# Optimization experiments

Measured on AMD Instinct MI355X. Metric: run time of the kernel, lower is better.

## Reference

```python
import jax, jax.numpy as jnp
import numpy as np

C = 1024
FACTOR = 4
C_INT = C * FACTOR


def setup_inputs() -> dict:
    key = jax.random.key(0)
    ks = jax.random.split(key, 6)
    act = jax.random.normal(ks[0], (4, 2048, C), dtype=jnp.float32)
    mask = jnp.ones((4, 2048), dtype=jnp.float32)
    # LayerNorm params
    ln_scale = jnp.ones((C,), dtype=jnp.float32)
    ln_bias = jnp.zeros((C,), dtype=jnp.float32)
    # Linear 1 (init='linear'): lecun-normal-ish
    w1 = jax.random.normal(ks[1], (C, C_INT), dtype=jnp.float32) / np.sqrt(C)
    b1 = jnp.zeros((C_INT,), dtype=jnp.float32)
    # Linear 2 (init='final' -> zeros in AF2; use small random so grads are nontrivial)
    w2 = jax.random.normal(ks[2], (C_INT, C), dtype=jnp.float32) * 0.02
    b2 = jnp.zeros((C,), dtype=jnp.float32)
    return {"act": act, "mask": mask, "ln_scale": ln_scale, "ln_bias": ln_bias,
            "w1": w1, "b1": b1, "w2": w2, "b2": b2}


def _layernorm(x, scale, bias, eps=1e-5):
    mu = jnp.mean(x, axis=-1, keepdims=True)
    var = jnp.mean(jnp.square(x - mu), axis=-1, keepdims=True)
    return (x - mu) * jax.lax.rsqrt(var + eps) * scale + bias


def reference(act, mask, ln_scale, ln_bias, w1, b1, w2, b2):
    # mask is accepted but unused, matching the original forward.
    x = _layernorm(act, ln_scale, ln_bias)
    h = jax.nn.relu(jnp.einsum('bsc,cf->bsf', x, w1) + b1)
    return jnp.einsum('bsf,fc->bsc', h, w2) + b2
```

## Files before the change

kernel.cpp:

```cpp
#include <hip/hip_runtime.h>
#include <hip/hip_bf16.h>
#include <cstdint>

typedef unsigned short u16;
typedef __bf16 bf16x8 __attribute__((ext_vector_type(8)));
typedef float floatx4 __attribute__((ext_vector_type(4)));

#define AS1 __attribute__((address_space(1)))
#define AS3 __attribute__((address_space(3)))

static __device__ __forceinline__ u16 f2bf(float f) {
    union { float f; unsigned int u; } v; v.f = f;
    unsigned int u = v.u;
    return (u16)((u + 0x7FFFu + ((u >> 16) & 1u)) >> 16);
}

__device__ __forceinline__ void transpose_body(
    const float* __restrict__ in, u16* __restrict__ out,
    int R, int Ccols, int bx, int by, int tid, float (*tile)[33])
{
    const int tx = tid & 31;
    const int ty = tid >> 5;
    const int c0 = bx * 32;
    const int r0 = by * 32;
#pragma unroll
    for (int i = 0; i < 32; i += 8)
        tile[ty + i][tx] = in[(size_t)(r0 + ty + i) * Ccols + (c0 + tx)];
    __syncthreads();
#pragma unroll
    for (int i = 0; i < 32; i += 8)
        out[(size_t)(c0 + ty + i) * R + (r0 + tx)] = f2bf(tile[tx][ty + i]);
}

__global__ __launch_bounds__(256)
void prep(const float* __restrict__ w1, const float* __restrict__ w2,
          const float* __restrict__ act, const float* __restrict__ ln_scale,
          const float* __restrict__ ln_bias,
          u16* __restrict__ W1t, u16* __restrict__ W2t, u16* __restrict__ X)
{
    __shared__ float smem[32][33];
    const int id  = blockIdx.x;
    const int tid = threadIdx.x;

    if (id < 4096) {
        transpose_body(w1, W1t, 1024, 4096, id & 127, id >> 7, tid, smem);
        return;
    }
    if (id < 8192) {
        const int t = id - 4096;
        transpose_body(w2, W2t, 4096, 1024, t & 31, t >> 5, tid, smem);
        return;
    }
    const int row = id - 8192;
    const float4 v = ((const float4*)(act + (size_t)row * 1024))[tid];
    float s  = v.x + v.y + v.z + v.w;
    float ss = v.x * v.x + v.y * v.y + v.z * v.z + v.w * v.w;
#pragma unroll
    for (int off = 32; off > 0; off >>= 1) {
        s  += __shfl_xor(s, off, 64);
        ss += __shfl_xor(ss, off, 64);
    }
    float* red = &smem[0][0];
    const int wave = tid >> 6, lane = tid & 63;
    if (lane == 0) { red[wave] = s; red[4 + wave] = ss; }
    __syncthreads();
    s  = red[0] + red[1] + red[2] + red[3];
    ss = red[4] + red[5] + red[6] + red[7];
    const float mu  = s * (1.0f / 1024.0f);
    const float var = ss * (1.0f / 1024.0f) - mu * mu;
    const float rs  = rsqrtf(var + 1e-5f);
    const float4 sc = ((const float4*)ln_scale)[tid];
    const float4 bi = ((const float4*)ln_bias)[tid];
    ushort4 o;
    o.x = f2bf((v.x - mu) * rs * sc.x + bi.x);
    o.y = f2bf((v.y - mu) * rs * sc.y + bi.y);
    o.z = f2bf((v.z - mu) * rs * sc.z + bi.z);
    o.w = f2bf((v.w - mu) * rs * sc.w + bi.w);
    ((ushort4*)(X + (size_t)row * 1024))[tid] = o;
}

template <int BK, bool BF16_OUT, bool RELU>
__global__ __launch_bounds__(256)
void gemm_bt(const u16* __restrict__ A,
             const u16* __restrict__ Bt,
             const float* __restrict__ bias,
             void* __restrict__ Cout,
             int M, int N, int K)
{
    constexpr int SLOTS  = BK / 8;
    constexpr int RPI    = 64 / SLOTS;
    constexpr int IPW    = SLOTS / 2;
    constexpr int HALVES = BK / 32;

    __shared__ __align__(16) u16 Alds[128 * BK];
    __shared__ __align__(16) u16 Blds[128 * BK];

    const int tid  = threadIdx.x;
    const int wave = tid >> 6;
    const int lane = tid & 63;
    const int wm   = wave & 1;
    const int wn   = wave >> 1;
    const int quad = lane >> 4;
    const int l16  = lane & 15;

    const int nbm = M >> 7;
    const int id  = blockIdx.x;
    const int bm  = id % nbm;
    const int bn  = id / nbm;

    const u16* Ag = A  + (size_t)bm * 128 * K;
    const u16* Bg = Bt + (size_t)bn * 128 * K;

    const int srow = lane / SLOTS;
    const int s_st = lane & (SLOTS - 1);

    const int rkey = (SLOTS == 4) ? ((l16 >> 1) & 3) : (l16 & (SLOTS - 1));

    floatx4 acc[4][4];
#pragma unroll
    for (int i = 0; i < 4; ++i)
#pragma unroll
        for (int j = 0; j < 4; ++j)
            acc[i][j] = (floatx4){0.f, 0.f, 0.f, 0.f};

    for (int k0 = 0; k0 < K; k0 += BK) {
        __syncthreads();
#pragma unroll
        for (int r = 0; r < IPW; ++r) {
            const int chunk = wave * IPW + r;
            const int row = chunk * RPI + srow;
            const int key = (SLOTS == 4) ? ((row >> 1) & 3)
                                         : (row & (SLOTS - 1));
            const int scol = (s_st ^ key) * 8;
            __builtin_amdgcn_global_load_lds(
                (AS1 void*)(Ag + (size_t)row * K + k0 + scol),
                (AS3 void*)(&Alds[chunk * 512]), 16, 0, 0);
            __builtin_amdgcn_global_load_lds(
                (AS1 void*)(Bg + (size_t)row * K + k0 + scol),
                (AS3 void*)(&Blds[chunk * 512]), 16, 0, 0);
        }
        __syncthreads();

#pragma unroll
        for (int h = 0; h < HALVES; ++h) {
            const int slot = ((quad + 4 * h) ^ rkey) * 8;
            bf16x8 bfr[4];
#pragma unroll
            for (int ni = 0; ni < 4; ++ni) {
                const int brow = wn * 64 + ni * 16 + l16;
                bfr[ni] = *(const bf16x8*)(&Blds[brow * BK + slot]);
            }
#pragma unroll
            for (int mi = 0; mi < 4; ++mi) {
                const int arow = wm * 64 + mi * 16 + l16;
                const bf16x8 a = *(const bf16x8*)(&Alds[arow * BK + slot]);
#pragma unroll
                for (int ni = 0; ni < 4; ++ni)
                    acc[mi][ni] = __builtin_amdgcn_mfma_f32_16x16x32_bf16(
                        bfr[ni], a, acc[mi][ni], 0, 0, 0);
            }
        }
    }

    const int mbase = bm * 128 + wm * 64;
    const int nbase = bn * 128 + wn * 64;
#pragma unroll
    for (int mi = 0; mi < 4; ++mi) {
        const int m = mbase + mi * 16 + l16;
#pragma unroll
        for (int ni = 0; ni < 4; ++ni) {
            const int n0 = nbase + ni * 16 + quad * 4;
            const float4 bv = *(const float4*)&bias[n0];
            float v0 = acc[mi][ni][0] + bv.x;
            float v1 = acc[mi][ni][1] + bv.y;
            float v2 = acc[mi][ni][2] + bv.z;
            float v3 = acc[mi][ni][3] + bv.w;
            if (RELU) {
                v0 = fmaxf(v0, 0.f); v1 = fmaxf(v1, 0.f);
                v2 = fmaxf(v2, 0.f); v3 = fmaxf(v3, 0.f);
            }
            if (BF16_OUT) {
                ushort4 o = { f2bf(v0), f2bf(v1), f2bf(v2), f2bf(v3) };
                *(ushort4*)&((u16*)Cout)[(size_t)m * N + n0] = o;
            } else {
                float4 o = { v0, v1, v2, v3 };
                *(float4*)&((float*)Cout)[(size_t)m * N + n0] = o;
            }
        }
    }
}

extern "C" void kernel_launch(void* const* d_in, const int* in_sizes, int n_in,
                              void* d_out, int out_size, void* d_ws, size_t ws_size,
                              hipStream_t stream)
{
    const float* act      = (const float*)d_in[0];
    const float* ln_scale = (const float*)d_in[2];
    const float* ln_bias  = (const float*)d_in[3];
    const float* w1       = (const float*)d_in[4];
    const float* b1       = (const float*)d_in[5];
    const float* w2       = (const float*)d_in[6];
    const float* b2       = (const float*)d_in[7];
    float* out = (float*)d_out;

    const int M = 8192, C = 1024, CI = 4096;

    u16* X   = (u16*)d_ws;
    u16* W1t = X   + (size_t)M * C;
    u16* W2t = W1t + (size_t)CI * C;
    u16* H   = W2t + (size_t)C * CI;

    prep<<<16384, 256, 0, stream>>>(w1, w2, act, ln_scale, ln_bias, W1t, W2t, X);
    gemm_bt<64, true, true><<<(M / 128) * (CI / 128), 256, 0, stream>>>(
        X, W1t, b1, (void*)H, M, CI, C);
    gemm_bt<128, false, false><<<(M / 128) * (C / 128), 256, 0, stream>>>(
        H, W2t, b2, (void*)out, M, C, CI);
}
```

Before: 268.0 us.

## Rewrite GEMMs with 256x128 tiles and triple-buffered async LDS pipeline

Replaces the 128x128 single-buffered GEMM with a 256x128-tile, 512-thread kernel that uses three LDS buffers. It prefetches two k-tiles ahead with global_load_lds, so memory loads overlap the MFMA work. Explicit vmcnt waits, sched barriers and setprio control the interleaving. The larger tile raises reuse per block, but it uses more LDS and needs more registers per block, and the hand-placed waits risk synchronisation bugs.

```diff
diff --git a/kernel.cpp b/kernel.cpp
--- a/kernel.cpp
+++ b/kernel.cpp
@@ -13,6 +13,14 @@
     union { float f; unsigned int u; } v; v.f = f;
     unsigned int u = v.u;
     return (u16)((u + 0x7FFFu + ((u >> 16) & 1u)) >> 16);
+}
+
+static __device__ __forceinline__ void bar() {
+    __builtin_amdgcn_sched_barrier(0);
+    asm volatile("" ::: "memory");
+    __builtin_amdgcn_s_barrier();
+    asm volatile("" ::: "memory");
+    __builtin_amdgcn_sched_barrier(0);
 }
 
 __device__ __forceinline__ void transpose_body(
@@ -79,42 +87,55 @@
     ((ushort4*)(X + (size_t)row * 1024))[tid] = o;
 }
 
-template <int BK, bool BF16_OUT, bool RELU>
-__global__ __launch_bounds__(256)
-void gemm_bt(const u16* __restrict__ A,
+template <bool BF16_OUT, bool RELU>
+__global__ __launch_bounds__(512, 2)
+void gemm256(const u16* __restrict__ A,
              const u16* __restrict__ Bt,
              const float* __restrict__ bias,
              void* __restrict__ Cout,
              int M, int N, int K)
 {
-    constexpr int SLOTS  = BK / 8;
-    constexpr int RPI    = 64 / SLOTS;
-    constexpr int IPW    = SLOTS / 2;
-    constexpr int HALVES = BK / 32;
-
-    __shared__ __align__(16) u16 Alds[128 * BK];
-    __shared__ __align__(16) u16 Blds[128 * BK];
+    constexpr int BM = 256, BN = 128, BK = 64;
+    constexpr int ASZ = BM * BK;
+    constexpr int BSZ = BN * BK;
+    __shared__ __align__(16) u16 Alds[3 * ASZ];
+    __shared__ __align__(16) u16 Blds[3 * BSZ];
 
     const int tid  = threadIdx.x;
     const int wave = tid >> 6;
     const int lane = tid & 63;
-    const int wm   = wave & 1;
-    const int wn   = wave >> 1;
+    const int srow = lane >> 3;
+    const int s_st = lane & 7;
     const int quad = lane >> 4;
     const int l16  = lane & 15;
-
-    const int nbm = M >> 7;
+    const int rkey = l16 & 7;
+    const int wm   = wave >> 1;
+    const int wn   = wave & 1;
+
+    const int nbm = M >> 8;
     const int id  = blockIdx.x;
     const int bm  = id % nbm;
     const int bn  = id / nbm;
 
-    const u16* Ag = A  + (size_t)bm * 128 * K;
-    const u16* Bg = Bt + (size_t)bn * 128 * K;
-
-    const int srow = lane / SLOTS;
-    const int s_st = lane & (SLOTS - 1);
-
-    const int rkey = (SLOTS == 4) ? ((l16 >> 1) & 3) : (l16 & (SLOTS - 1));
+    const u16* Ag = A  + (size_t)bm * BM * K;
+    const u16* Bg = Bt + (size_t)bn * BN * K;
+
+    auto stageA = [&](int r, int k0, int ab) {
+        const int ca  = wave * 4 + r;
+        const int row = ca * 8 + srow;
+        const int col = (s_st ^ (row & 7)) * 8;
+        __builtin_amdgcn_global_load_lds(
+            (AS1 void*)(Ag + (size_t)row * K + k0 + col),
+            (AS3 void*)(&Alds[ab + ca * 512]), 16, 0, 0);
+    };
+    auto stageB = [&](int r, int k0, int bb) {
+        const int cb  = wave * 2 + r;
+        const int row = cb * 8 + srow;
+        const int col = (s_st ^ (row & 7)) * 8;
+        __builtin_amdgcn_global_load_lds(
+            (AS1 void*)(Bg + (size_t)row * K + k0 + col),
+            (AS3 void*)(&Blds[bb + cb * 512]), 16, 0, 0);
+    };
 
     floatx4 acc[4][4];
 #pragma unroll
@@ -123,47 +144,67 @@
         for (int j = 0; j < 4; ++j)
             acc[i][j] = (floatx4){0.f, 0.f, 0.f, 0.f};
 
-    for (int k0 = 0; k0 < K; k0 += BK) {
-        __syncthreads();
-#pragma unroll
-        for (int r = 0; r < IPW; ++r) {
-            const int chunk = wave * IPW + r;
-            const int row = chunk * RPI + srow;
-            const int key = (SLOTS == 4) ? ((row >> 1) & 3)
-                                         : (row & (SLOTS - 1));
-            const int scol = (s_st ^ key) * 8;
-            __builtin_amdgcn_global_load_lds(
-                (AS1 void*)(Ag + (size_t)row * K + k0 + scol),
-                (AS3 void*)(&Alds[chunk * 512]), 16, 0, 0);
-            __builtin_amdgcn_global_load_lds(
-                (AS1 void*)(Bg + (size_t)row * K + k0 + scol),
-                (AS3 void*)(&Blds[chunk * 512]), 16, 0, 0);
-        }
-        __syncthreads();
-
-#pragma unroll
-        for (int h = 0; h < HALVES; ++h) {
-            const int slot = ((quad + 4 * h) ^ rkey) * 8;
-            bf16x8 bfr[4];
-#pragma unroll
-            for (int ni = 0; ni < 4; ++ni) {
-                const int brow = wn * 64 + ni * 16 + l16;
-                bfr[ni] = *(const bf16x8*)(&Blds[brow * BK + slot]);
-            }
-#pragma unroll
-            for (int mi = 0; mi < 4; ++mi) {
-                const int arow = wm * 64 + mi * 16 + l16;
-                const bf16x8 a = *(const bf16x8*)(&Alds[arow * BK + slot]);
+    const int NT = K >> 6;
+
+#pragma unroll
+    for (int r = 0; r < 4; ++r) stageA(r, 0, 0);
+#pragma unroll
+    for (int r = 0; r < 2; ++r) stageB(r, 0, 0);
+#pragma unroll
+    for (int r = 0; r < 4; ++r) stageA(r, BK, ASZ);
+#pragma unroll
+    for (int r = 0; r < 2; ++r) stageB(r, BK, BSZ);
+    asm volatile("s_waitcnt vmcnt(6)" ::: "memory");
+    bar();
+
+    int bsel = 0;
+    for (int t = 0; t < NT; ++t) {
+        const int ab  = bsel * ASZ;
+        const int bb  = bsel * BSZ;
+        const int bs2 = (bsel >= 1) ? bsel - 1 : 2;
+        const int ab2 = bs2 * ASZ;
+        const int bb2 = bs2 * BSZ;
+        const bool do_stage = (t + 2 < NT);
+        const int  k2 = (t + 2) << 6;
+
+#pragma unroll
+        for (int kk = 0; kk < 2; ++kk) {
+            const int slot = ((kk * 4 + quad) ^ rkey) * 8;
+            bf16x8 afr[4], bfr[4];
+#pragma unroll
+            for (int i = 0; i < 4; ++i) {
+                afr[i] = *(const bf16x8*)
+                    &Alds[ab + (wm * 64 + i * 16 + l16) * 64 + slot];
+                bfr[i] = *(const bf16x8*)
+                    &Blds[bb + (wn * 64 + i * 16 + l16) * 64 + slot];
+            }
+            if (do_stage) {
+                stageA(kk * 2 + 0, k2, ab2);
+                stageA(kk * 2 + 1, k2, ab2);
+                stageB(kk, k2, bb2);
+            }
+            bar();
+            __builtin_amdgcn_s_setprio(1);
+#pragma unroll
+            for (int mi = 0; mi < 4; ++mi)
 #pragma unroll
                 for (int ni = 0; ni < 4; ++ni)
                     acc[mi][ni] = __builtin_amdgcn_mfma_f32_16x16x32_bf16(
-                        bfr[ni], a, acc[mi][ni], 0, 0, 0);
-            }
+                        bfr[ni], afr[mi], acc[mi][ni], 0, 0, 0);
+            __builtin_amdgcn_s_setprio(0);
+            if (kk == 1) {
+                if (do_stage)
+                    asm volatile("s_waitcnt vmcnt(6)" ::: "memory");
+                else if (t + 1 < NT)
+                    asm volatile("s_waitcnt vmcnt(0)" ::: "memory");
+            }
+            bar();
         }
-    }
-
-    const int mbase = bm * 128 + wm * 64;
-    const int nbase = bn * 128 + wn * 64;
+        bsel = (bsel == 2) ? 0 : bsel + 1;
+    }
+
+    const int mbase = bm * BM + wm * 64;
+    const int nbase = bn * BN + wn * 64;
 #pragma unroll
     for (int mi = 0; mi < 4; ++mi) {
         const int m = mbase + mi * 16 + l16;
@@ -211,8 +252,8 @@
     u16* H   = W2t + (size_t)C * CI;
 
     prep<<<16384, 256, 0, stream>>>(w1, w2, act, ln_scale, ln_bias, W1t, W2t, X);
-    gemm_bt<64, true, true><<<(M / 128) * (CI / 128), 256, 0, stream>>>(
+    gemm256<true, true><<<(M / 256) * (CI / 128), 512, 0, stream>>>(
         X, W1t, b1, (void*)H, M, CI, C);
-    gemm_bt<128, false, false><<<(M / 128) * (C / 128), 256, 0, stream>>>(
+    gemm256<false, false><<<(M / 256) * (C / 128), 512, 0, stream>>>(
         H, W2t, b2, (void*)out, M, C, CI);
 }
```

Result: slower. 278.4 us (+3.9%).

## Rewrite both GEMMs with larger tiles and double-buffered LDS pipelining

Applied to the files above, without the earlier changes.

Replaces the generic single-buffered GEMM with two specialized kernels. Each uses 512-thread blocks, larger output tiles (256x256 for the first GEMM, 256x128 for the second), and double-buffered LDS. Global-to-LDS loads for the next K tile are interleaved with MFMA phases, controlled by explicit waitcnt, barriers, sched_barrier and setprio. The aim is to hide global load latency and improve data reuse, at the cost of more registers and LDS per block and hand-tuned scheduling that is fragile.

```diff
diff --git a/kernel.cpp b/kernel.cpp
--- a/kernel.cpp
+++ b/kernel.cpp
@@ -8,6 +8,9 @@
 
 #define AS1 __attribute__((address_space(1)))
 #define AS3 __attribute__((address_space(3)))
+
+#define SCHED0  __builtin_amdgcn_sched_barrier(0)
+#define BARRIER __builtin_amdgcn_s_barrier()
 
 static __device__ __forceinline__ u16 f2bf(float f) {
     union { float f; unsigned int u; } v; v.f = f;
@@ -79,113 +82,251 @@
     ((ushort4*)(X + (size_t)row * 1024))[tid] = o;
 }
 
-template <int BK, bool BF16_OUT, bool RELU>
-__global__ __launch_bounds__(256)
-void gemm_bt(const u16* __restrict__ A,
-             const u16* __restrict__ Bt,
-             const float* __restrict__ bias,
-             void* __restrict__ Cout,
-             int M, int N, int K)
-{
-    constexpr int SLOTS  = BK / 8;
-    constexpr int RPI    = 64 / SLOTS;
-    constexpr int IPW    = SLOTS / 2;
-    constexpr int HALVES = BK / 32;
-
-    __shared__ __align__(16) u16 Alds[128 * BK];
-    __shared__ __align__(16) u16 Blds[128 * BK];
+__global__ __launch_bounds__(512, 2)
+void gemm1(const u16* __restrict__ A, const u16* __restrict__ Bt,
+           const float* __restrict__ bias, u16* __restrict__ H)
+{
+    constexpr int K = 1024, N = 4096;
+    constexpr int ASZ = 256 * 64;
+    __shared__ __align__(16) u16 Alds[2 * ASZ];
+    __shared__ __align__(16) u16 Blds[2 * ASZ];
 
     const int tid  = threadIdx.x;
     const int wave = tid >> 6;
     const int lane = tid & 63;
-    const int wm   = wave & 1;
-    const int wn   = wave >> 1;
+    const int srow = lane >> 3;
+    const int sst  = lane & 7;
     const int quad = lane >> 4;
     const int l16  = lane & 15;
-
-    const int nbm = M >> 7;
-    const int id  = blockIdx.x;
-    const int bm  = id % nbm;
-    const int bn  = id / nbm;
-
-    const u16* Ag = A  + (size_t)bm * 128 * K;
-    const u16* Bg = Bt + (size_t)bn * 128 * K;
-
-    const int srow = lane / SLOTS;
-    const int s_st = lane & (SLOTS - 1);
-
-    const int rkey = (SLOTS == 4) ? ((l16 >> 1) & 3) : (l16 & (SLOTS - 1));
-
-    floatx4 acc[4][4];
-#pragma unroll
-    for (int i = 0; i < 4; ++i)
+    const int rkey = l16 & 7;
+    const int wm   = wave >> 2;
+    const int wn   = wave & 3;
+
+    const int id = blockIdx.x;
+    const int bm = id & 31;
+    const int bn = id >> 5;
+
+    const u16* Ag = A  + (size_t)bm * 256 * K;
+    const u16* Bg = Bt + (size_t)bn * 256 * K;
+
+    auto stA = [&](int buf, int c, int k0) {
+        const int row = c * 64 + wave * 8 + srow;
+        const int col = (sst ^ (row & 7)) * 8;
+        __builtin_amdgcn_global_load_lds(
+            (AS1 void*)(Ag + (size_t)row * K + k0 + col),
+            (AS3 void*)(&Alds[buf * ASZ + c * 4096 + wave * 512]), 16, 0, 0);
+    };
+    auto stB = [&](int buf, int c, int k0) {
+        const int row = c * 64 + wave * 8 + srow;
+        const int col = (sst ^ (row & 7)) * 8;
+        __builtin_amdgcn_global_load_lds(
+            (AS1 void*)(Bg + (size_t)row * K + k0 + col),
+            (AS3 void*)(&Blds[buf * ASZ + c * 4096 + wave * 512]), 16, 0, 0);
+    };
+
+    floatx4 acc[8][4];
+#pragma unroll
+    for (int i = 0; i < 8; ++i)
 #pragma unroll
         for (int j = 0; j < 4; ++j)
             acc[i][j] = (floatx4){0.f, 0.f, 0.f, 0.f};
 
-    for (int k0 = 0; k0 < K; k0 += BK) {
-        __syncthreads();
-#pragma unroll
-        for (int r = 0; r < IPW; ++r) {
-            const int chunk = wave * IPW + r;
-            const int row = chunk * RPI + srow;
-            const int key = (SLOTS == 4) ? ((row >> 1) & 3)
-                                         : (row & (SLOTS - 1));
-            const int scol = (s_st ^ key) * 8;
-            __builtin_amdgcn_global_load_lds(
-                (AS1 void*)(Ag + (size_t)row * K + k0 + scol),
-                (AS3 void*)(&Alds[chunk * 512]), 16, 0, 0);
-            __builtin_amdgcn_global_load_lds(
-                (AS1 void*)(Bg + (size_t)row * K + k0 + scol),
-                (AS3 void*)(&Blds[chunk * 512]), 16, 0, 0);
+    constexpr int NT = K / 64;
+
+    stA(0, 0, 0); stA(0, 2, 0);
+    stB(0, 0, 0); stB(0, 1, 0); stB(0, 2, 0); stB(0, 3, 0);
+    stA(0, 1, 0); stA(0, 3, 0);
+    asm volatile("s_waitcnt vmcnt(2)" ::: "memory");
+    SCHED0; BARRIER; SCHED0;
+
+    bf16x8 bres[4][2];
+    for (int t = 0; t < NT; ++t) {
+        const int cb = t & 1, nb = cb ^ 1;
+        const int ab = cb * ASZ, bb = cb * ASZ;
+        const int k1 = (t + 1) * 64;
+        const bool st = (t + 1 < NT);
+
+#pragma unroll
+        for (int p = 0; p < 4; ++p) {
+            if (p == 0) {
+#pragma unroll
+                for (int ni = 0; ni < 4; ++ni) {
+                    const int br = wn * 64 + ni * 16 + l16;
+#pragma unroll
+                    for (int kh = 0; kh < 2; ++kh)
+                        bres[ni][kh] = *(const bf16x8*)
+                            &Blds[bb + br * 64 + ((kh * 4 + quad) ^ rkey) * 8];
+                }
+            }
+            bf16x8 afr[2][2];
+#pragma unroll
+            for (int j = 0; j < 2; ++j) {
+                const int ar = wm * 128 + (2 * p + j) * 16 + l16;
+#pragma unroll
+                for (int kh = 0; kh < 2; ++kh)
+                    afr[j][kh] = *(const bf16x8*)
+                        &Alds[ab + ar * 64 + ((kh * 4 + quad) ^ rkey) * 8];
+            }
+            if (st) {
+                if (p == 0)      { stA(nb, 0, k1); stA(nb, 2, k1); }
+                else if (p == 1) { stB(nb, 0, k1); stB(nb, 1, k1); }
+                else if (p == 2) { stB(nb, 2, k1); stB(nb, 3, k1); }
+                else             { stA(nb, 1, k1); stA(nb, 3, k1); }
+            }
+            SCHED0; BARRIER;
+            asm volatile("s_waitcnt lgkmcnt(0)" ::: "memory");
+            SCHED0;
+            __builtin_amdgcn_s_setprio(1);
+#pragma unroll
+            for (int kh = 0; kh < 2; ++kh)
+#pragma unroll
+                for (int j = 0; j < 2; ++j)
+#pragma unroll
+                    for (int ni = 0; ni < 4; ++ni)
+                        acc[2 * p + j][ni] = __builtin_amdgcn_mfma_f32_16x16x32_bf16(
+                            bres[ni][kh], afr[j][kh], acc[2 * p + j][ni], 0, 0, 0);
+            __builtin_amdgcn_s_setprio(0);
+            SCHED0;
+            if (p == 1) {
+                if (st) asm volatile("s_waitcnt vmcnt(4)" ::: "memory");
+                else    asm volatile("s_waitcnt vmcnt(0)" ::: "memory");
+            }
+            if (p == 3 && st)
+                asm volatile("s_waitcnt vmcnt(2)" ::: "memory");
+            BARRIER; SCHED0;
         }
-        __syncthreads();
-
-#pragma unroll
-        for (int h = 0; h < HALVES; ++h) {
-            const int slot = ((quad + 4 * h) ^ rkey) * 8;
-            bf16x8 bfr[4];
-#pragma unroll
-            for (int ni = 0; ni < 4; ++ni) {
-                const int brow = wn * 64 + ni * 16 + l16;
-                bfr[ni] = *(const bf16x8*)(&Blds[brow * BK + slot]);
-            }
-#pragma unroll
-            for (int mi = 0; mi < 4; ++mi) {
-                const int arow = wm * 64 + mi * 16 + l16;
-                const bf16x8 a = *(const bf16x8*)(&Alds[arow * BK + slot]);
-#pragma unroll
-                for (int ni = 0; ni < 4; ++ni)
-                    acc[mi][ni] = __builtin_amdgcn_mfma_f32_16x16x32_bf16(
-                        bfr[ni], a, acc[mi][ni], 0, 0, 0);
-            }
-        }
-    }
-
-    const int mbase = bm * 128 + wm * 64;
-    const int nbase = bn * 128 + wn * 64;
-#pragma unroll
-    for (int mi = 0; mi < 4; ++mi) {
+    }
+
+    const int mbase = bm * 256 + wm * 128;
+    const int nbase = bn * 256 + wn * 64;
+#pragma unroll
+    for (int mi = 0; mi < 8; ++mi) {
         const int m = mbase + mi * 16 + l16;
 #pragma unroll
         for (int ni = 0; ni < 4; ++ni) {
             const int n0 = nbase + ni * 16 + quad * 4;
             const float4 bv = *(const float4*)&bias[n0];
-            float v0 = acc[mi][ni][0] + bv.x;
-            float v1 = acc[mi][ni][1] + bv.y;
-            float v2 = acc[mi][ni][2] + bv.z;
-            float v3 = acc[mi][ni][3] + bv.w;
-            if (RELU) {
-                v0 = fmaxf(v0, 0.f); v1 = fmaxf(v1, 0.f);
-                v2 = fmaxf(v2, 0.f); v3 = fmaxf(v3, 0.f);
-            }
-            if (BF16_OUT) {
-                ushort4 o = { f2bf(v0), f2bf(v1), f2bf(v2), f2bf(v3) };
-                *(ushort4*)&((u16*)Cout)[(size_t)m * N + n0] = o;
-            } else {
-                float4 o = { v0, v1, v2, v3 };
-                *(float4*)&((float*)Cout)[(size_t)m * N + n0] = o;
-            }
+            float v0 = fmaxf(acc[mi][ni][0] + bv.x, 0.f);
+            float v1 = fmaxf(acc[mi][ni][1] + bv.y, 0.f);
+            float v2 = fmaxf(acc[mi][ni][2] + bv.z, 0.f);
+            float v3 = fmaxf(acc[mi][ni][3] + bv.w, 0.f);
+            ushort4 o = { f2bf(v0), f2bf(v1), f2bf(v2), f2bf(v3) };
+            *(ushort4*)&H[(size_t)m * N + n0] = o;
+        }
+    }
+}
+
+__global__ __launch_bounds__(512, 2)
+void gemm2(const u16* __restrict__ A, const u16* __restrict__ Bt,
+           const float* __restrict__ bias, float* __restrict__ Cout)
+{
+    constexpr int K = 4096, N = 1024;
+    constexpr int ASZ = 2 * 256 * 32;
+    constexpr int BSZ = 2 * 128 * 32;
+    __shared__ __align__(16) u16 Alds[2 * ASZ];
+    __shared__ __align__(16) u16 Blds[2 * BSZ];
+
+    const int tid  = threadIdx.x;
+    const int wave = tid >> 6;
+    const int lane = tid & 63;
+    const int quad = lane >> 4;
+    const int l16  = lane & 15;
+    const int key4 = (l16 >> 1) & 3;
+    const int wm   = wave >> 1;
+    const int wn   = wave & 1;
+
+    const int id = blockIdx.x;
+    const int bm = id & 31;
+    const int bn = id >> 5;
+
+    const u16* Ag = A  + (size_t)bm * 256 * K;
+    const u16* Bg = Bt + (size_t)bn * 128 * K;
+
+    auto stA = [&](int buf, int kh, int c, int k0) {
+        const int row = c * 128 + wave * 16 + (lane >> 2);
+        const int col = kh * 32 + ((lane & 3) ^ ((row >> 1) & 3)) * 8;
+        __builtin_amdgcn_global_load_lds(
+            (AS1 void*)(Ag + (size_t)row * K + k0 + col),
+            (AS3 void*)(&Alds[buf * ASZ + kh * 8192 + c * 4096 + wave * 512]),
+            16, 0, 0);
+    };
+    auto stB = [&](int buf, int kh, int k0) {
+        const int row = wave * 16 + (lane >> 2);
+        const int col = kh * 32 + ((lane & 3) ^ ((row >> 1) & 3)) * 8;
+        __builtin_amdgcn_global_load_lds(
+            (AS1 void*)(Bg + (size_t)row * K + k0 + col),
+            (AS3 void*)(&Blds[buf * BSZ + kh * 4096 + wave * 512]), 16, 0, 0);
+    };
+
+    floatx4 acc[4][4];
+#pragma unroll
+    for (int i = 0; i < 4; ++i)
+#pragma unroll
+        for (int j = 0; j < 4; ++j)
+            acc[i][j] = (floatx4){0.f, 0.f, 0.f, 0.f};
+
+    constexpr int NT = K / 64;
+
+    stA(0, 0, 0, 0); stA(0, 0, 1, 0); stB(0, 0, 0);
+    stA(0, 1, 0, 0); stA(0, 1, 1, 0); stB(0, 1, 0);
+    asm volatile("s_waitcnt vmcnt(3)" ::: "memory");
+    SCHED0; BARRIER; SCHED0;
+
+    for (int t = 0; t < NT; ++t) {
+        const int cb = t & 1, nb = cb ^ 1;
+        const int k1 = (t + 1) * 64;
+        const bool st = (t + 1 < NT);
+
+#pragma unroll
+        for (int kh = 0; kh < 2; ++kh) {
+            bf16x8 afr[4], bfr[4];
+#pragma unroll
+            for (int mi = 0; mi < 4; ++mi) {
+                const int ar = wm * 64 + mi * 16 + l16;
+                afr[mi] = *(const bf16x8*)
+                    &Alds[cb * ASZ + kh * 8192 + ar * 32 + ((quad ^ key4) * 8)];
+            }
+#pragma unroll
+            for (int ni = 0; ni < 4; ++ni) {
+                const int br = wn * 64 + ni * 16 + l16;
+                bfr[ni] = *(const bf16x8*)
+                    &Blds[cb * BSZ + kh * 4096 + br * 32 + ((quad ^ key4) * 8)];
+            }
+            if (st) { stA(nb, kh, 0, k1); stA(nb, kh, 1, k1); stB(nb, kh, k1); }
+            SCHED0; BARRIER;
+            asm volatile("s_waitcnt lgkmcnt(0)" ::: "memory");
+            SCHED0;
+            __builtin_amdgcn_s_setprio(1);
+#pragma unroll
+            for (int mi = 0; mi < 4; ++mi)
+#pragma unroll
+                for (int ni = 0; ni < 4; ++ni)
+                    acc[mi][ni] = __builtin_amdgcn_mfma_f32_16x16x32_bf16(
+                        bfr[ni], afr[mi], acc[mi][ni], 0, 0, 0);
+            __builtin_amdgcn_s_setprio(0);
+            SCHED0;
+            if (kh == 0) {
+                if (st) asm volatile("s_waitcnt vmcnt(3)" ::: "memory");
+                else    asm volatile("s_waitcnt vmcnt(0)" ::: "memory");
+            } else if (st) {
+                asm volatile("s_waitcnt vmcnt(3)" ::: "memory");
+            }
+            BARRIER; SCHED0;
+        }
+    }
+
+    const int mbase = bm * 256 + wm * 64;
+    const int nbase = bn * 128 + wn * 64;
+#pragma unroll
+    for (int mi = 0; mi < 4; ++mi) {
+        const int m = mbase + mi * 16 + l16;
+#pragma unroll
+        for (int ni = 0; ni < 4; ++ni) {
+            const int n0 = nbase + ni * 16 + quad * 4;
+            const float4 bv = *(const float4*)&bias[n0];
+            float4 o = { acc[mi][ni][0] + bv.x, acc[mi][ni][1] + bv.y,
+                         acc[mi][ni][2] + bv.z, acc[mi][ni][3] + bv.w };
+            *(float4*)&Cout[(size_t)m * N + n0] = o;
         }
     }
 }
@@ -211,8 +352,6 @@
     u16* H   = W2t + (size_t)C * CI;
 
     prep<<<16384, 256, 0, stream>>>(w1, w2, act, ln_scale, ln_bias, W1t, W2t, X);
-    gemm_bt<64, true, true><<<(M / 128) * (CI / 128), 256, 0, stream>>>(
-        X, W1t, b1, (void*)H, M, CI, C);
-    gemm_bt<128, false, false><<<(M / 128) * (C / 128), 256, 0, stream>>>(
-        H, W2t, b2, (void*)out, M, C, CI);
-}
+    gemm1<<<(M / 256) * (CI / 256), 512, 0, stream>>>(X, W1t, b1, H);
+    gemm2<<<(M / 256) * (C / 128), 512, 0, stream>>>(H, W2t, b2, out);
+}
```

After: 268.2 us. Within noise of the previous version (+0.1%).
